# Kernel tuning notes

Hardware: AMD Instinct MI355X
Metric: run time of the kernel (lower is better)

## Reference

```python
import jax, jax.numpy as jnp
import numpy as np

DIM = 2048
N_HEADS = 16
N_KV = 4
HEAD_DIM = DIM // N_HEADS  # 128
B, S = 2, 2048
EPS = float(np.finfo(np.float32).eps)  # torch RMSNorm eps=None -> finfo eps


def _rotate_half(x):
    # interleaved-pair rotation: out[..., ::2] = -x[..., 1::2]; out[..., 1::2] = x[..., ::2]
    x2 = x.reshape(x.shape[:-1] + (HEAD_DIM // 2, 2))
    rot = jnp.stack([-x2[..., 1], x2[..., 0]], axis=-1)
    return rot.reshape(x.shape)


def _rmsnorm(x, w):
    var = jnp.mean(x * x, axis=-1, keepdims=True)
    return x * jax.lax.rsqrt(var + EPS) * w


def setup_inputs() -> dict:
    key = jax.random.key(0)
    ks = jax.random.split(key, 5)
    out_f = (N_HEADS + 2 * N_KV) * HEAD_DIM  # 3072
    return {
        "x": jax.random.normal(ks[0], (B, S, DIM), jnp.float32),
        "wqkv": jax.random.normal(ks[1], (out_f, DIM), jnp.float32) * (2.0 / (DIM + out_f)) ** 0.5,
        "wo": jax.random.normal(ks[2], (DIM, DIM), jnp.float32) * (1.0 / DIM) ** 0.5,
        "q_norm_w": jnp.ones((HEAD_DIM,), jnp.float32),
        "k_norm_w": jnp.ones((HEAD_DIM,), jnp.float32),
        "freqs_cos": jnp.cos(jax.random.normal(ks[3], (S, 1, HEAD_DIM), jnp.float32)),
        "freqs_sin": jnp.sin(jax.random.normal(ks[4], (S, 1, HEAD_DIM), jnp.float32)),
    }


def reference(x, wqkv, wo, q_norm_w, k_norm_w, freqs_cos, freqs_sin):
    b, s, _ = x.shape
    qkv = jnp.einsum("bsd,od->bso", x, wqkv)
    q_size = N_HEADS * HEAD_DIM
    kv_size = N_KV * HEAD_DIM
    xq = qkv[..., :q_size].reshape(b, s, N_HEADS, HEAD_DIM)
    xk = qkv[..., q_size:q_size + kv_size].reshape(b, s, N_KV, HEAD_DIM)
    xv = qkv[..., q_size + kv_size:].reshape(b, s, N_KV, HEAD_DIM)
    xq = _rmsnorm(xq, q_norm_w)
    xk = _rmsnorm(xk, k_norm_w)
    # RoPE (freqs broadcast over batch and heads)
    xq = xq * freqs_cos + _rotate_half(xq) * freqs_sin
    xk = xk * freqs_cos + _rotate_half(xk) * freqs_sin
    # GQA: group query heads per kv head instead of materializing repeats
    rep = N_HEADS // N_KV
    q = xq.transpose(0, 2, 1, 3).reshape(b, N_KV, rep, s, HEAD_DIM)
    k = xk.transpose(0, 2, 1, 3)  # [b, kv, s, d]
    v = xv.transpose(0, 2, 1, 3)
    scale = 1.0 / jnp.sqrt(jnp.asarray(HEAD_DIM, x.dtype))
    scores = jnp.einsum("bhgqd,bhkd->bhgqk", q, k) * scale
    probs = jax.nn.softmax(scores, axis=-1)
    attn = jnp.einsum("bhgqk,bhkd->bhgqd", probs, v)
    attn = attn.reshape(b, N_HEADS, s, HEAD_DIM).transpose(0, 2, 1, 3).reshape(b, s, DIM)
    return jnp.einsum("bsd,od->bso", attn, wo)
```

## Files before the change

### kernel.cpp

```cpp
#include <hip/hip_runtime.h>
#include <hip/hip_bf16.h>

typedef unsigned short u16;
typedef __bf16 bf16x8 __attribute__((ext_vector_type(8)));
typedef __bf16 bf16x4 __attribute__((ext_vector_type(4)));
typedef u16 u16x8 __attribute__((ext_vector_type(8)));
typedef float f32x4 __attribute__((ext_vector_type(4)));
typedef float f32x16 __attribute__((ext_vector_type(16)));

__device__ __forceinline__ u16 f2bf(float f) {
    unsigned u = __float_as_uint(f);
    return (u16)((u + 0x7fffu + ((u >> 16) & 1u)) >> 16);
}
__device__ __forceinline__ unsigned pkbf2(float a, float b) {
    __hip_bfloat162 h = __float22bfloat162_rn(make_float2(a, b));
    return *(unsigned*)&h;
}

__global__ void cvt_bf16(const float* __restrict__ src, u16* __restrict__ dst, int n4) {
    int i = blockIdx.x * 256 + threadIdx.x;
    if (i >= n4) return;
    float4 v = *(const float4*)(src + (size_t)i * 4);
    uint2 o; o.x = pkbf2(v.x, v.y); o.y = pkbf2(v.z, v.w);
    *(uint2*)(dst + (size_t)i * 4) = o;
}

__device__ __forceinline__ void gemm_core(const u16* __restrict__ Ab,
                                          const u16* __restrict__ Bb, int K,
                                          f32x4 acc[4][4], int wave, int lane) {
    __shared__ u16 As[2][128 * 32];
    __shared__ u16 Bs[2][128 * 32];
    const int quad = lane >> 4, l16 = lane & 15;
    const int wr = (wave >> 1) * 64, wc = (wave & 1) * 64;
    const int strow = lane >> 2;
    const int stk = (lane & 3) * 8;

    const u16* pa0 = Ab + (size_t)(wave * 32 + strow) * K + stk;
    const u16* pa1 = pa0 + (size_t)16 * K;
    const u16* pb0 = Bb + (size_t)(wave * 32 + strow) * K + stk;
    const u16* pb1 = pb0 + (size_t)16 * K;
    const int lrow0 = (wave * 32 + strow) * 32 + stk;
    const int lrow1 = (wave * 32 + 16 + strow) * 32 + stk;

    u16x8 a0 = *(const u16x8*)pa0, a1 = *(const u16x8*)pa1;
    u16x8 b0 = *(const u16x8*)pb0, b1 = *(const u16x8*)pb1;
    *(u16x8*)&As[0][lrow0] = a0; *(u16x8*)&As[0][lrow1] = a1;
    *(u16x8*)&Bs[0][lrow0] = b0; *(u16x8*)&Bs[0][lrow1] = b1;
    __syncthreads();

    const int nk = K >> 5;
    for (int kt = 0; kt < nk; ++kt) {
        const int cur = kt & 1, nxt = cur ^ 1;
        if (kt + 1 < nk) {
            const int off = (kt + 1) * 32;
            a0 = *(const u16x8*)(pa0 + off); a1 = *(const u16x8*)(pa1 + off);
            b0 = *(const u16x8*)(pb0 + off); b1 = *(const u16x8*)(pb1 + off);
        }
        bf16x8 af[4], bfr[4];
#pragma unroll
        for (int mt = 0; mt < 4; ++mt)
            af[mt] = *(const bf16x8*)&As[cur][(wr + mt * 16 + l16) * 32 + quad * 8];
#pragma unroll
        for (int nt = 0; nt < 4; ++nt)
            bfr[nt] = *(const bf16x8*)&Bs[cur][(wc + nt * 16 + l16) * 32 + quad * 8];
#pragma unroll
        for (int mt = 0; mt < 4; ++mt)
#pragma unroll
            for (int nt = 0; nt < 4; ++nt)
                acc[mt][nt] = __builtin_amdgcn_mfma_f32_16x16x32_bf16(
                    af[mt], bfr[nt], acc[mt][nt], 0, 0, 0);
        if (kt + 1 < nk) {
            *(u16x8*)&As[nxt][lrow0] = a0; *(u16x8*)&As[nxt][lrow1] = a1;
            *(u16x8*)&Bs[nxt][lrow0] = b0; *(u16x8*)&Bs[nxt][lrow1] = b1;
        }
        __syncthreads();
    }
}

__global__ __launch_bounds__(256)
void gemm_bt(const u16* __restrict__ A, const u16* __restrict__ B,
             float* __restrict__ C, int M, int N, int K) {
    const int tid = threadIdx.x, wave = tid >> 6, lane = tid & 63;
    const int quad = lane >> 4, l16 = lane & 15;
    const int wr = (wave >> 1) * 64, wc = (wave & 1) * 64;
    const size_t bm = (size_t)blockIdx.y * 128, bn = (size_t)blockIdx.x * 128;
    f32x4 acc[4][4] = {};
    gemm_core(A + bm * K, B + bn * K, K, acc, wave, lane);
#pragma unroll
    for (int mt = 0; mt < 4; ++mt)
#pragma unroll
        for (int nt = 0; nt < 4; ++nt)
#pragma unroll
            for (int r = 0; r < 4; ++r)
                C[(bm + wr + mt * 16 + quad * 4 + r) * (size_t)N + bn + wc + nt * 16 + l16] =
                    acc[mt][nt][r];
}

__global__ __launch_bounds__(256)
void gemm_qkv(const u16* __restrict__ xb, const u16* __restrict__ wq,
              const float* __restrict__ qw, const float* __restrict__ kw,
              const float* __restrict__ fcos, const float* __restrict__ fsin,
              u16* __restrict__ qb, u16* __restrict__ kb, u16* __restrict__ vt) {
    const int tid = threadIdx.x, wave = tid >> 6, lane = tid & 63;
    const int quad = lane >> 4, l16 = lane & 15;
    const int wr = (wave >> 1) * 64, wc = (wave & 1) * 64;
    const int tn = blockIdx.x, bmb = blockIdx.y;
    f32x4 acc[4][4] = {};
    gemm_core(xb + (size_t)bmb * 128 * 2048, wq + (size_t)tn * 128 * 2048, 2048,
              acc, wave, lane);

    const int b = bmb >> 4;
    const int sbase = (bmb & 15) * 128 + wr;

    if (tn >= 20) {
        const int kv = tn - 20;
        u16* base = vt + (size_t)(b * 4 + kv) * 128 * 2048;
#pragma unroll
        for (int mt = 0; mt < 4; ++mt) {
            int s0 = sbase + mt * 16 + quad * 4;
#pragma unroll
            for (int nt = 0; nt < 4; ++nt) {
                int col = wc + nt * 16 + l16;
                bf16x4 pv;
#pragma unroll
                for (int r = 0; r < 4; ++r) pv[r] = (__bf16)acc[mt][nt][r];
                *(bf16x4*)(base + (size_t)col * 2048 + s0) = pv;
            }
        }
        return;
    }

    __shared__ float red[2][128];
    float ssq[4][4];
#pragma unroll
    for (int mt = 0; mt < 4; ++mt)
#pragma unroll
        for (int r = 0; r < 4; ++r) {
            float t = 0.f;
#pragma unroll
            for (int nt = 0; nt < 4; ++nt) t += acc[mt][nt][r] * acc[mt][nt][r];
#pragma unroll
            for (int off = 1; off <= 8; off <<= 1) t += __shfl_xor(t, off);
            ssq[mt][r] = t;
        }
    if (l16 == 0)
#pragma unroll
        for (int mt = 0; mt < 4; ++mt)
#pragma unroll
            for (int r = 0; r < 4; ++r)
                red[wave & 1][wr + mt * 16 + quad * 4 + r] = ssq[mt][r];
    __syncthreads();

    const float qscl = (tn < 16) ? 0.08838834764831845f * 1.4426950408889634f : 1.0f;
    const float* wp = (tn < 16) ? qw : kw;
    float wcol[4];
#pragma unroll
    for (int nt = 0; nt < 4; ++nt) wcol[nt] = wp[wc + nt * 16 + l16];
    u16* dstbase = (tn < 16) ? qb + (size_t)(b * 16 + tn) * 2048 * 128
                             : kb + (size_t)(b * 4 + (tn - 16)) * 2048 * 128;
    const float sgn = (l16 & 1) ? 1.f : -1.f;

#pragma unroll
    for (int mt = 0; mt < 4; ++mt) {
#pragma unroll
        for (int r = 0; r < 4; ++r) {
            int row = wr + mt * 16 + quad * 4 + r;
            float var = (red[0][row] + red[1][row]) * (1.0f / 128.0f);
            float rms = rsqrtf(var + 1.1920928955078125e-07f) * qscl;
            int s = sbase + mt * 16 + quad * 4 + r;
            const float* fc = fcos + (size_t)s * 128 + wc;
            const float* fn = fsin + (size_t)s * 128 + wc;
            u16* drow = dstbase + (size_t)s * 128 + wc;
#pragma unroll
            for (int nt = 0; nt < 4; ++nt) {
                float y = acc[mt][nt][r] * rms * wcol[nt];
                float yp = __shfl_xor(y, 1);
                float o = y * fc[nt * 16 + l16] + sgn * yp * fn[nt * 16 + l16];
                drow[nt * 16 + l16] = f2bf(o);
            }
        }
    }
}

#define KBUF(c) ((c) * 8192)
#define VBUF(c) (16384 + (c) * 8192)
__global__ __launch_bounds__(256, 2)
void flash_attn(const u16* __restrict__ qb, const u16* __restrict__ kb,
                const u16* __restrict__ vt, u16* __restrict__ ab) {
    __shared__ u16 smem[32768];
    __shared__ float Llds[128];

    const int tid = threadIdx.x;
    const int wave = tid >> 6, lane = tid & 63;
    const int hf = lane >> 5, c32 = lane & 31;
    const int qt = blockIdx.x, hh = blockIdx.y, bb = blockIdx.z;
    const int kh = hh >> 2;

    const u16* Qbase = qb + (size_t)(bb * 16 + hh) * 2048 * 128;
    const u16* Kbase = kb + (size_t)(bb * 4 + kh) * 2048 * 128;
    const u16* Vbase = vt + (size_t)(bb * 4 + kh) * 128 * 2048;

    bf16x8 aq[8];
#pragma unroll
    for (int kq = 0; kq < 8; ++kq)
        aq[kq] = *(const bf16x8*)(Qbase +
            (size_t)(qt * 128 + wave * 32 + c32) * 128 + kq * 16 + hf * 8);

    f32x16 O[4] = {};
    float lacc = 0.f;

    const int st_key = tid >> 4, st_c16 = tid & 15;
    const int st_d = tid >> 3, st_c8 = tid & 7;

    u16x8 kreg[4], vreg[4];
#pragma unroll
    for (int it = 0; it < 4; ++it) {
        int key = st_key + it * 16, d = st_d + it * 32;
        kreg[it] = *(const u16x8*)(Kbase + (size_t)key * 128 + st_c16 * 8);
        vreg[it] = *(const u16x8*)(Vbase + (size_t)d * 2048 + st_c8 * 8);
    }
#pragma unroll
    for (int it = 0; it < 4; ++it) {
        int key = st_key + it * 16, d = st_d + it * 32;
        *(u16x8*)&smem[KBUF(0) + key * 128 + ((st_c16 ^ (key & 7)) * 8)] = kreg[it];
        *(u16x8*)&smem[VBUF(0) + d * 64 + ((st_c8 ^ (d & 7)) * 8)] = vreg[it];
    }
    __syncthreads();

    for (int kt = 0; kt < 32; ++kt) {
        const int cur = kt & 1, nxt = cur ^ 1;
        if (kt < 31) {
            const int key0n = (kt + 1) * 64;
#pragma unroll
            for (int it = 0; it < 4; ++it) {
                int key = st_key + it * 16, d = st_d + it * 32;
                kreg[it] = *(const u16x8*)(Kbase + (size_t)(key0n + key) * 128 + st_c16 * 8);
                vreg[it] = *(const u16x8*)(Vbase + (size_t)d * 2048 + key0n + st_c8 * 8);
            }
        }

        f32x16 sc[2] = {};
#pragma unroll
        for (int kq = 0; kq < 8; ++kq) {
#pragma unroll
            for (int mt = 0; mt < 2; ++mt) {
                bf16x8 kf = *(const bf16x8*)&smem[KBUF(cur) + (mt * 32 + c32) * 128 +
                                                 (((kq * 2 + hf) ^ (c32 & 7)) * 8)];
                sc[mt] = __builtin_amdgcn_mfma_f32_32x32x16_bf16(kf, aq[kq], sc[mt], 0, 0, 0);
            }
        }

        int pdw[2][8];
#pragma unroll
        for (int mt = 0; mt < 2; ++mt) {
            float p[16];
#pragma unroll
            for (int r = 0; r < 16; ++r) {
                p[r] = __builtin_amdgcn_exp2f(sc[mt][r]);
                lacc += p[r];
            }
#pragma unroll
            for (int i = 0; i < 8; ++i) pdw[mt][i] = (int)pkbf2(p[2 * i], p[2 * i + 1]);
        }

        if (kt < 31) {
#pragma unroll
            for (int it = 0; it < 4; ++it) {
                int key = st_key + it * 16, d = st_d + it * 32;
                *(u16x8*)&smem[KBUF(nxt) + key * 128 + ((st_c16 ^ (key & 7)) * 8)] = kreg[it];
                *(u16x8*)&smem[VBUF(nxt) + d * 64 + ((st_c8 ^ (d & 7)) * 8)] = vreg[it];
            }
        }

#pragma unroll
        for (int kc = 0; kc < 4; ++kc) {
            const int mt = kc >> 1, L = kc & 1;
            int s0 = hf ? pdw[mt][4 * L + 0] : pdw[mt][4 * L + 2];
            int s1 = hf ? pdw[mt][4 * L + 1] : pdw[mt][4 * L + 3];
            int r0 = __shfl_xor(s0, 32);
            int r1 = __shfl_xor(s1, 32);
            union { int i[4]; bf16x8 v; } u;
            u.i[0] = hf ? r0 : pdw[mt][4 * L + 0];
            u.i[1] = hf ? r1 : pdw[mt][4 * L + 1];
            u.i[2] = hf ? pdw[mt][4 * L + 2] : r0;
            u.i[3] = hf ? pdw[mt][4 * L + 3] : r1;
#pragma unroll
            for (int dt = 0; dt < 4; ++dt) {
                bf16x8 vf = *(const bf16x8*)&smem[VBUF(cur) + (dt * 32 + c32) * 64 +
                                                 (((kc * 2 + hf) ^ (c32 & 7)) * 8)];
                O[dt] = __builtin_amdgcn_mfma_f32_32x32x16_bf16(u.v, vf, O[dt], 0, 0, 0);
            }
        }
        __syncthreads();
    }

    float l = lacc + __shfl_xor(lacc, 32);
    if (hf == 0) Llds[wave * 32 + c32] = l;

    float inv[16];
#pragma unroll
    for (int r = 0; r < 16; ++r)
        inv[r] = __builtin_amdgcn_rcpf(Llds[wave * 32 + (r & 3) + 8 * (r >> 2) + 4 * hf]);

    u16* scr = &smem[wave * 32 * 136];
#pragma unroll
    for (int dt = 0; dt < 4; ++dt)
#pragma unroll
        for (int r = 0; r < 16; ++r) {
            int q_r = (r & 3) + 8 * (r >> 2) + 4 * hf;
            scr[q_r * 136 + dt * 32 + c32] = f2bf(O[dt][r] * inv[r]);
        }
#pragma unroll
    for (int it = 0; it < 8; ++it) {
        int f = it * 64 + lane;
        int row = f >> 4, c = f & 15;
        u16x8 v = *(const u16x8*)&scr[row * 136 + c * 8];
        int qg = qt * 128 + wave * 32 + row;
        *(u16x8*)(ab + ((size_t)(bb * 2048 + qg)) * 2048 + hh * 128 + c * 8) = v;
    }
}

extern "C" void kernel_launch(void* const* d_in, const int* in_sizes, int n_in,
                              void* d_out, int out_size, void* d_ws, size_t ws_size,
                              hipStream_t stream) {
    const float* x    = (const float*)d_in[0];
    const float* wqkv = (const float*)d_in[1];
    const float* wo   = (const float*)d_in[2];
    const float* qw   = (const float*)d_in[3];
    const float* kw   = (const float*)d_in[4];
    const float* fc   = (const float*)d_in[5];
    const float* fs   = (const float*)d_in[6];
    float* out = (float*)d_out;
    char* ws = (char*)d_ws;

    u16* xb    = (u16*)(ws + 0);
    u16* wqkvb = (u16*)(ws + 16777216);
    u16* wob   = (u16*)(ws + 29360128);
    u16* qb    = (u16*)(ws + 37748736);
    u16* kb    = (u16*)(ws + 54525952);
    u16* vt    = (u16*)(ws + 58720256);
    u16* ab    = (u16*)(ws + 62914560);

    cvt_bf16<<<8192, 256, 0, stream>>>(x, xb, 2097152);
    cvt_bf16<<<6144, 256, 0, stream>>>(wqkv, wqkvb, 1572864);
    cvt_bf16<<<4096, 256, 0, stream>>>(wo, wob, 1048576);
    gemm_qkv<<<dim3(24, 32), 256, 0, stream>>>(xb, wqkvb, qw, kw, fc, fs, qb, kb, vt);
    flash_attn<<<dim3(16, 16, 2), 256, 0, stream>>>(qb, kb, vt, ab);
    gemm_bt<<<dim3(16, 32), 256, 0, stream>>>(ab, wob, out, 4096, 2048, 2048);
}
```

Before: 333.3 us.

## Enlarge GEMM tiles to 256x128 with padded LDS rows

Both GEMMs (QKV projection and output projection) now use 256x128 block tiles, with each wave computing 128x64 through 8x4 MFMA accumulators. The grids are halved to match. LDS rows are padded to a stride of 40 elements to cut bank conflicts on the fragment reads, and launch bounds request 2 blocks per SM. The aim is more arithmetic per byte loaded and fewer LDS conflicts. The cost is more accumulator registers and fewer blocks: 384 and 256 blocks across 256 CUs, which can leave wave quantization imbalance.

```diff
diff --git a/kernel.cpp b/kernel.cpp
--- a/kernel.cpp
+++ b/kernel.cpp
@@ -25,27 +25,42 @@
     *(uint2*)(dst + (size_t)i * 4) = o;
 }
 
-__device__ __forceinline__ void gemm_core(const u16* __restrict__ Ab,
-                                          const u16* __restrict__ Bb, int K,
-                                          f32x4 acc[4][4], int wave, int lane) {
-    __shared__ u16 As[2][128 * 32];
-    __shared__ u16 Bs[2][128 * 32];
+#define LSTR 40
+__device__ __forceinline__ void gemm_core256(const u16* __restrict__ Ab,
+                                             const u16* __restrict__ Bb, int K,
+                                             f32x4 acc[8][4], int tid) {
+    __shared__ u16 As[2][256 * LSTR];
+    __shared__ u16 Bs[2][128 * LSTR];
+    const int wave = tid >> 6, lane = tid & 63;
     const int quad = lane >> 4, l16 = lane & 15;
-    const int wr = (wave >> 1) * 64, wc = (wave & 1) * 64;
-    const int strow = lane >> 2;
-    const int stk = (lane & 3) * 8;
-
-    const u16* pa0 = Ab + (size_t)(wave * 32 + strow) * K + stk;
-    const u16* pa1 = pa0 + (size_t)16 * K;
-    const u16* pb0 = Bb + (size_t)(wave * 32 + strow) * K + stk;
-    const u16* pb1 = pb0 + (size_t)16 * K;
-    const int lrow0 = (wave * 32 + strow) * 32 + stk;
-    const int lrow1 = (wave * 32 + 16 + strow) * 32 + stk;
-
-    u16x8 a0 = *(const u16x8*)pa0, a1 = *(const u16x8*)pa1;
-    u16x8 b0 = *(const u16x8*)pb0, b1 = *(const u16x8*)pb1;
-    *(u16x8*)&As[0][lrow0] = a0; *(u16x8*)&As[0][lrow1] = a1;
-    *(u16x8*)&Bs[0][lrow0] = b0; *(u16x8*)&Bs[0][lrow1] = b1;
+    const int wr = (wave >> 1) * 128, wc = (wave & 1) * 64;
+    const int strow = tid >> 2;
+    const int stk = (tid & 3) * 8;
+
+    const u16* pa[4]; int la[4];
+#pragma unroll
+    for (int p = 0; p < 4; ++p) {
+        int row = p * 64 + strow;
+        pa[p] = Ab + (size_t)row * K + stk;
+        la[p] = row * LSTR + stk;
+    }
+    const u16* pb[2]; int lb[2];
+#pragma unroll
+    for (int p = 0; p < 2; ++p) {
+        int row = p * 64 + strow;
+        pb[p] = Bb + (size_t)row * K + stk;
+        lb[p] = row * LSTR + stk;
+    }
+
+    u16x8 ar[4], br[2];
+#pragma unroll
+    for (int p = 0; p < 4; ++p) ar[p] = *(const u16x8*)pa[p];
+#pragma unroll
+    for (int p = 0; p < 2; ++p) br[p] = *(const u16x8*)pb[p];
+#pragma unroll
+    for (int p = 0; p < 4; ++p) *(u16x8*)&As[0][la[p]] = ar[p];
+#pragma unroll
+    for (int p = 0; p < 2; ++p) *(u16x8*)&Bs[0][lb[p]] = br[p];
     __syncthreads();
 
     const int nk = K >> 5;
@@ -53,41 +68,45 @@
         const int cur = kt & 1, nxt = cur ^ 1;
         if (kt + 1 < nk) {
             const int off = (kt + 1) * 32;
-            a0 = *(const u16x8*)(pa0 + off); a1 = *(const u16x8*)(pa1 + off);
-            b0 = *(const u16x8*)(pb0 + off); b1 = *(const u16x8*)(pb1 + off);
-        }
-        bf16x8 af[4], bfr[4];
-#pragma unroll
-        for (int mt = 0; mt < 4; ++mt)
-            af[mt] = *(const bf16x8*)&As[cur][(wr + mt * 16 + l16) * 32 + quad * 8];
+#pragma unroll
+            for (int p = 0; p < 4; ++p) ar[p] = *(const u16x8*)(pa[p] + off);
+#pragma unroll
+            for (int p = 0; p < 2; ++p) br[p] = *(const u16x8*)(pb[p] + off);
+        }
+        bf16x8 af[8], bfr[4];
+#pragma unroll
+        for (int mt = 0; mt < 8; ++mt)
+            af[mt] = *(const bf16x8*)&As[cur][(wr + mt * 16 + l16) * LSTR + quad * 8];
 #pragma unroll
         for (int nt = 0; nt < 4; ++nt)
-            bfr[nt] = *(const bf16x8*)&Bs[cur][(wc + nt * 16 + l16) * 32 + quad * 8];
-#pragma unroll
-        for (int mt = 0; mt < 4; ++mt)
+            bfr[nt] = *(const bf16x8*)&Bs[cur][(wc + nt * 16 + l16) * LSTR + quad * 8];
+#pragma unroll
+        for (int mt = 0; mt < 8; ++mt)
 #pragma unroll
             for (int nt = 0; nt < 4; ++nt)
                 acc[mt][nt] = __builtin_amdgcn_mfma_f32_16x16x32_bf16(
                     af[mt], bfr[nt], acc[mt][nt], 0, 0, 0);
         if (kt + 1 < nk) {
-            *(u16x8*)&As[nxt][lrow0] = a0; *(u16x8*)&As[nxt][lrow1] = a1;
-            *(u16x8*)&Bs[nxt][lrow0] = b0; *(u16x8*)&Bs[nxt][lrow1] = b1;
+#pragma unroll
+            for (int p = 0; p < 4; ++p) *(u16x8*)&As[nxt][la[p]] = ar[p];
+#pragma unroll
+            for (int p = 0; p < 2; ++p) *(u16x8*)&Bs[nxt][lb[p]] = br[p];
         }
         __syncthreads();
     }
 }
 
-__global__ __launch_bounds__(256)
+__global__ __launch_bounds__(256, 2)
 void gemm_bt(const u16* __restrict__ A, const u16* __restrict__ B,
              float* __restrict__ C, int M, int N, int K) {
     const int tid = threadIdx.x, wave = tid >> 6, lane = tid & 63;
     const int quad = lane >> 4, l16 = lane & 15;
-    const int wr = (wave >> 1) * 64, wc = (wave & 1) * 64;
-    const size_t bm = (size_t)blockIdx.y * 128, bn = (size_t)blockIdx.x * 128;
-    f32x4 acc[4][4] = {};
-    gemm_core(A + bm * K, B + bn * K, K, acc, wave, lane);
-#pragma unroll
-    for (int mt = 0; mt < 4; ++mt)
+    const int wr = (wave >> 1) * 128, wc = (wave & 1) * 64;
+    const size_t bm = (size_t)blockIdx.y * 256, bn = (size_t)blockIdx.x * 128;
+    f32x4 acc[8][4] = {};
+    gemm_core256(A + bm * K, B + bn * K, K, acc, tid);
+#pragma unroll
+    for (int mt = 0; mt < 8; ++mt)
 #pragma unroll
         for (int nt = 0; nt < 4; ++nt)
 #pragma unroll
@@ -96,27 +115,27 @@
                     acc[mt][nt][r];
 }
 
-__global__ __launch_bounds__(256)
+__global__ __launch_bounds__(256, 2)
 void gemm_qkv(const u16* __restrict__ xb, const u16* __restrict__ wq,
               const float* __restrict__ qw, const float* __restrict__ kw,
               const float* __restrict__ fcos, const float* __restrict__ fsin,
               u16* __restrict__ qb, u16* __restrict__ kb, u16* __restrict__ vt) {
     const int tid = threadIdx.x, wave = tid >> 6, lane = tid & 63;
     const int quad = lane >> 4, l16 = lane & 15;
-    const int wr = (wave >> 1) * 64, wc = (wave & 1) * 64;
+    const int wr = (wave >> 1) * 128, wc = (wave & 1) * 64;
     const int tn = blockIdx.x, bmb = blockIdx.y;
-    f32x4 acc[4][4] = {};
-    gemm_core(xb + (size_t)bmb * 128 * 2048, wq + (size_t)tn * 128 * 2048, 2048,
-              acc, wave, lane);
-
-    const int b = bmb >> 4;
-    const int sbase = (bmb & 15) * 128 + wr;
+    f32x4 acc[8][4] = {};
+    gemm_core256(xb + (size_t)bmb * 256 * 2048, wq + (size_t)tn * 128 * 2048, 2048,
+                 acc, tid);
+
+    const int b = bmb >> 3;
+    const int sbase = (bmb & 7) * 256 + wr;
 
     if (tn >= 20) {
         const int kv = tn - 20;
         u16* base = vt + (size_t)(b * 4 + kv) * 128 * 2048;
 #pragma unroll
-        for (int mt = 0; mt < 4; ++mt) {
+        for (int mt = 0; mt < 8; ++mt) {
             int s0 = sbase + mt * 16 + quad * 4;
 #pragma unroll
             for (int nt = 0; nt < 4; ++nt) {
@@ -130,10 +149,10 @@
         return;
     }
 
-    __shared__ float red[2][128];
-    float ssq[4][4];
-#pragma unroll
-    for (int mt = 0; mt < 4; ++mt)
+    __shared__ float red[2][256];
+    float ssq;
+#pragma unroll
+    for (int mt = 0; mt < 8; ++mt)
 #pragma unroll
         for (int r = 0; r < 4; ++r) {
             float t = 0.f;
@@ -141,14 +160,8 @@
             for (int nt = 0; nt < 4; ++nt) t += acc[mt][nt][r] * acc[mt][nt][r];
 #pragma unroll
             for (int off = 1; off <= 8; off <<= 1) t += __shfl_xor(t, off);
-            ssq[mt][r] = t;
-        }
-    if (l16 == 0)
-#pragma unroll
-        for (int mt = 0; mt < 4; ++mt)
-#pragma unroll
-            for (int r = 0; r < 4; ++r)
-                red[wave & 1][wr + mt * 16 + quad * 4 + r] = ssq[mt][r];
+            if (l16 == 0) red[wave & 1][wr + mt * 16 + quad * 4 + r] = t;
+        }
     __syncthreads();
 
     const float qscl = (tn < 16) ? 0.08838834764831845f * 1.4426950408889634f : 1.0f;
@@ -161,7 +174,7 @@
     const float sgn = (l16 & 1) ? 1.f : -1.f;
 
 #pragma unroll
-    for (int mt = 0; mt < 4; ++mt) {
+    for (int mt = 0; mt < 8; ++mt) {
 #pragma unroll
         for (int r = 0; r < 4; ++r) {
             int row = wr + mt * 16 + quad * 4 + r;
@@ -344,7 +357,7 @@
     cvt_bf16<<<8192, 256, 0, stream>>>(x, xb, 2097152);
     cvt_bf16<<<6144, 256, 0, stream>>>(wqkv, wqkvb, 1572864);
     cvt_bf16<<<4096, 256, 0, stream>>>(wo, wob, 1048576);
-    gemm_qkv<<<dim3(24, 32), 256, 0, stream>>>(xb, wqkvb, qw, kw, fc, fs, qb, kb, vt);
+    gemm_qkv<<<dim3(24, 16), 256, 0, stream>>>(xb, wqkvb, qw, kw, fc, fs, qb, kb, vt);
     flash_attn<<<dim3(16, 16, 2), 256, 0, stream>>>(qb, kb, vt, ab);
-    gemm_bt<<<dim3(16, 32), 256, 0, stream>>>(ab, wob, out, 4096, 2048, 2048);
-}
+    gemm_bt<<<dim3(16, 16), 256, 0, stream>>>(ab, wob, out, 4096, 2048, 2048);
+}
```

After: 335.6 us. No clear change (+0.7%).

## Use direct global-to-LDS loads in GEMM core, single-buffered

Applied to the files above, without the earlier changes.

Replaces the register-staged, double-buffered LDS loading in the shared GEMM core with __builtin_amdgcn_global_load_lds direct copies into a single LDS buffer, with barriers before and after each K-step. This cuts VGPR use and LDS size and removes the separate store instructions. In exchange, global loads no longer overlap the MFMA work of the previous tile, which may expose memory latency. It also writes the RMSNorm sum-of-squares partials to shared memory inside the reduction loop instead of through a temporary array.

```diff
diff --git a/kernel.cpp b/kernel.cpp
--- a/kernel.cpp
+++ b/kernel.cpp
@@ -28,52 +28,42 @@
 __device__ __forceinline__ void gemm_core(const u16* __restrict__ Ab,
                                           const u16* __restrict__ Bb, int K,
                                           f32x4 acc[4][4], int wave, int lane) {
-    __shared__ u16 As[2][128 * 32];
-    __shared__ u16 Bs[2][128 * 32];
+    __shared__ u16 As[128 * 32];
+    __shared__ u16 Bs[128 * 32];
     const int quad = lane >> 4, l16 = lane & 15;
     const int wr = (wave >> 1) * 64, wc = (wave & 1) * 64;
-    const int strow = lane >> 2;
+    const int strow = wave * 32 + (lane >> 2);
     const int stk = (lane & 3) * 8;
 
-    const u16* pa0 = Ab + (size_t)(wave * 32 + strow) * K + stk;
-    const u16* pa1 = pa0 + (size_t)16 * K;
-    const u16* pb0 = Bb + (size_t)(wave * 32 + strow) * K + stk;
-    const u16* pb1 = pb0 + (size_t)16 * K;
-    const int lrow0 = (wave * 32 + strow) * 32 + stk;
-    const int lrow1 = (wave * 32 + 16 + strow) * 32 + stk;
-
-    u16x8 a0 = *(const u16x8*)pa0, a1 = *(const u16x8*)pa1;
-    u16x8 b0 = *(const u16x8*)pb0, b1 = *(const u16x8*)pb1;
-    *(u16x8*)&As[0][lrow0] = a0; *(u16x8*)&As[0][lrow1] = a1;
-    *(u16x8*)&Bs[0][lrow0] = b0; *(u16x8*)&Bs[0][lrow1] = b1;
-    __syncthreads();
-
-    const int nk = K >> 5;
-    for (int kt = 0; kt < nk; ++kt) {
-        const int cur = kt & 1, nxt = cur ^ 1;
-        if (kt + 1 < nk) {
-            const int off = (kt + 1) * 32;
-            a0 = *(const u16x8*)(pa0 + off); a1 = *(const u16x8*)(pa1 + off);
-            b0 = *(const u16x8*)(pb0 + off); b1 = *(const u16x8*)(pb1 + off);
-        }
+    for (int k0 = 0; k0 < K; k0 += 32) {
+        __syncthreads();
+#pragma unroll
+        for (int c = 0; c < 2; ++c) {
+            const u16* ga = Ab + (size_t)(strow + c * 16) * K + k0 + stk;
+            const u16* gb = Bb + (size_t)(strow + c * 16) * K + k0 + stk;
+            __builtin_amdgcn_global_load_lds(
+                (__attribute__((address_space(1))) void*)ga,
+                (__attribute__((address_space(3))) void*)&As[(wave * 32 + c * 16) * 32],
+                16, 0, 0);
+            __builtin_amdgcn_global_load_lds(
+                (__attribute__((address_space(1))) void*)gb,
+                (__attribute__((address_space(3))) void*)&Bs[(wave * 32 + c * 16) * 32],
+                16, 0, 0);
+        }
+        __syncthreads();
         bf16x8 af[4], bfr[4];
 #pragma unroll
         for (int mt = 0; mt < 4; ++mt)
-            af[mt] = *(const bf16x8*)&As[cur][(wr + mt * 16 + l16) * 32 + quad * 8];
+            af[mt] = *(const bf16x8*)&As[(wr + mt * 16 + l16) * 32 + quad * 8];
 #pragma unroll
         for (int nt = 0; nt < 4; ++nt)
-            bfr[nt] = *(const bf16x8*)&Bs[cur][(wc + nt * 16 + l16) * 32 + quad * 8];
+            bfr[nt] = *(const bf16x8*)&Bs[(wc + nt * 16 + l16) * 32 + quad * 8];
 #pragma unroll
         for (int mt = 0; mt < 4; ++mt)
 #pragma unroll
             for (int nt = 0; nt < 4; ++nt)
                 acc[mt][nt] = __builtin_amdgcn_mfma_f32_16x16x32_bf16(
                     af[mt], bfr[nt], acc[mt][nt], 0, 0, 0);
-        if (kt + 1 < nk) {
-            *(u16x8*)&As[nxt][lrow0] = a0; *(u16x8*)&As[nxt][lrow1] = a1;
-            *(u16x8*)&Bs[nxt][lrow0] = b0; *(u16x8*)&Bs[nxt][lrow1] = b1;
-        }
-        __syncthreads();
     }
 }
 
@@ -131,7 +121,6 @@
     }
 
     __shared__ float red[2][128];
-    float ssq[4][4];
 #pragma unroll
     for (int mt = 0; mt < 4; ++mt)
 #pragma unroll
@@ -141,14 +130,8 @@
             for (int nt = 0; nt < 4; ++nt) t += acc[mt][nt][r] * acc[mt][nt][r];
 #pragma unroll
             for (int off = 1; off <= 8; off <<= 1) t += __shfl_xor(t, off);
-            ssq[mt][r] = t;
-        }
-    if (l16 == 0)
-#pragma unroll
-        for (int mt = 0; mt < 4; ++mt)
-#pragma unroll
-            for (int r = 0; r < 4; ++r)
-                red[wave & 1][wr + mt * 16 + quad * 4 + r] = ssq[mt][r];
+            if (l16 == 0) red[wave & 1][wr + mt * 16 + quad * 4 + r] = t;
+        }
     __syncthreads();
 
     const float qscl = (tn < 16) ? 0.08838834764831845f * 1.4426950408889634f : 1.0f;
```

Result: slower. 351.6 us (+5.5%).
